# Performance work log

Hardware: AMD Instinct MI355X
Metric: run time of the kernel (lower is better)

## Reference

```python
import jax, jax.numpy as jnp
import numpy as np

S_GRID = 14.0
L_COORD = 5.0
L_NOOBJ = 0.5
B = 2


def _xywh2xyxy(b):
    # b: [..., 4] with (x, y, w, h); x,y are divided by S per the original module
    xy = b[..., :2] / S_GRID
    wh = b[..., 2:4]
    return jnp.concatenate([xy - 0.5 * wh, xy + 0.5 * wh], axis=-1)


def setup_inputs() -> dict:
    key = jax.random.key(0)
    k1, k2, k3, k4 = jax.random.split(key, 4)
    N, S, C = 4096, 14, 20
    pred_tensor = jax.random.uniform(k1, (N, S, S, B * 5 + C), dtype=jnp.float32, minval=0.05, maxval=1.0)
    target_boxes = jax.random.uniform(k2, (N, S, S, 4), dtype=jnp.float32, minval=0.05, maxval=1.0)
    target_cls = jax.random.normal(k3, (N, S, S, C), dtype=jnp.float32)
    has_object_map = jax.random.randint(k4, (N, S, S), 0, 2).astype(jnp.bool_)
    return {"pred_tensor": pred_tensor, "target_boxes": target_boxes,
            "target_cls": target_cls, "has_object_map": has_object_map}


def reference(pred_tensor, target_boxes, target_cls, has_object_map):
    N = pred_tensor.shape[0]
    mask = has_object_map                      # [N,S,S] bool
    maskf = mask.astype(pred_tensor.dtype)
    pb = pred_tensor[..., :B * 5].reshape(*pred_tensor.shape[:3], B, 5)  # [N,S,S,B,5]
    pc = pred_tensor[..., B * 5:]              # [N,S,S,20]

    # class loss: masked sum of squared errors over classes
    cls_loss = jnp.sum(maskf * jnp.sum((target_cls - pc) ** 2, axis=-1))

    # no-object loss: conf^2 on cells without objects, summed over both boxes
    conf = pb[..., 4]                          # [N,S,S,B]
    no_obj_loss = L_NOOBJ * jnp.sum(jnp.where(~mask[..., None], conf, 0.0) ** 2)

    # per-cell IoU of target vs each of the B predicted boxes (diag of original NxM)
    t_xyxy = _xywh2xyxy(target_boxes)          # [N,S,S,4]
    p_xyxy = _xywh2xyxy(pb[..., :4])           # [N,S,S,B,4]
    lt = jnp.maximum(t_xyxy[..., None, :2], p_xyxy[..., :2])
    rb = jnp.minimum(t_xyxy[..., None, 2:], p_xyxy[..., 2:])
    wh = jnp.clip(rb - lt, 0.0)
    inter = wh[..., 0] * wh[..., 1]            # [N,S,S,B]
    area_t = (t_xyxy[..., 2] - t_xyxy[..., 0]) * (t_xyxy[..., 3] - t_xyxy[..., 1])
    area_p = (p_xyxy[..., 2] - p_xyxy[..., 0]) * (p_xyxy[..., 3] - p_xyxy[..., 1])
    iou = inter / (area_t[..., None] + area_p - inter)  # [N,S,S,B]

    best_iou = jnp.max(iou, axis=-1)           # [N,S,S]
    best_idx = jnp.argmax(iou, axis=-1)        # [N,S,S]
    best_box = jnp.take_along_axis(pb, best_idx[..., None, None], axis=3)[..., 0, :]  # [N,S,S,5]

    xy_diff = jnp.where(mask[..., None], best_box[..., :2] - target_boxes[..., :2], 0.0)
    wh_p = jnp.where(mask[..., None], best_box[..., 2:4], 1.0)
    wh_t = jnp.where(mask[..., None], target_boxes[..., 2:4], 1.0)
    reg_loss = L_COORD * (jnp.sum(xy_diff ** 2)
                          + jnp.sum((jnp.sqrt(wh_p) - jnp.sqrt(wh_t)) ** 2))

    # containing-object confidence loss: mse(best_iou, best_box_conf) on object cells
    containing_obj_loss = jnp.sum(jnp.where(mask, best_iou - best_box[..., 4], 0.0) ** 2)

    total_loss = (cls_loss + no_obj_loss + reg_loss + containing_obj_loss) / N
    return (total_loss, reg_loss, containing_obj_loss, no_obj_loss, cls_loss)
```

## Files before the change

### kernel.cpp

```cpp
#include <hip/hip_runtime.h>
#include <math.h>


#define BLOCK 256
#define WPB 4
#define CPW 64

__global__ __launch_bounds__(BLOCK) void k_yolo(
    const float*  __restrict__ pred,
    const float4* __restrict__ tbox4,
    const float4* __restrict__ tcls4,
    const int*    __restrict__ mask,
    float4*       __restrict__ partial,
    int n_cells)
{
    __shared__ float sp[WPB][CPW * 30];
    const int tid  = threadIdx.x;
    const int lane = tid & 63;
    const int w    = tid >> 6;
    const long long cell0 = ((long long)blockIdx.x * WPB + w) * CPW;

    float cls = 0.f, noobj = 0.f, reg = 0.f, cont = 0.f;

    int mflag = 0;
    if (cell0 < n_cells) {
        const float4* p4 = reinterpret_cast<const float4*>(pred + cell0 * 30);
        float4* s4 = reinterpret_cast<float4*>(sp[w]);
        #pragma unroll
        for (int i = 0; i < 8; ++i) {
            int k = lane + i * 64;
            if (k < 480) s4[k] = p4[k];
        }
        long long cell = cell0 + lane;
        if (cell < (long long)n_cells) mflag = mask[cell];
    }
    __syncthreads();

    if (cell0 + lane < (long long)n_cells) {
        const float2* pc2 = reinterpret_cast<const float2*>(sp[w] + lane * 30);
        float2 v0 = pc2[0], v1 = pc2[1], v2 = pc2[2], v3 = pc2[3], v4 = pc2[4];
        float4 tb = tbox4[cell0 + lane];
        if (mflag) {
            float txc = tb.x / 14.0f, tyc = tb.y / 14.0f;
            float t0 = txc - 0.5f * tb.z, t1 = tyc - 0.5f * tb.w;
            float t2 = txc + 0.5f * tb.z, t3 = tyc + 0.5f * tb.w;
            float area_t = (t2 - t0) * (t3 - t1);
            float bx[2] = { v0.x, v2.y }, by[2] = { v0.y, v3.x };
            float bw[2] = { v1.x, v3.y }, bh[2] = { v1.y, v4.x };
            float bcf[2] = { v2.x, v4.y };
            float iou[2];
            #pragma unroll
            for (int b = 0; b < 2; ++b) {
                float px = bx[b] / 14.0f, py = by[b] / 14.0f;
                float q0 = px - 0.5f * bw[b], q1 = py - 0.5f * bh[b];
                float q2 = px + 0.5f * bw[b], q3 = py + 0.5f * bh[b];
                float lt0 = fmaxf(t0, q0), lt1 = fmaxf(t1, q1);
                float rb0 = fminf(t2, q2), rb1 = fminf(t3, q3);
                float ww = fmaxf(rb0 - lt0, 0.f), hh = fmaxf(rb1 - lt1, 0.f);
                float inter = ww * hh;
                float area_p = (q2 - q0) * (q3 - q1);
                iou[b] = inter / (area_t + area_p - inter);
            }
            int bi = (iou[1] > iou[0]) ? 1 : 0;
            float dx = bx[bi] - tb.x, dy = by[bi] - tb.y;
            float swd = sqrtf(bw[bi]) - sqrtf(tb.z);
            float shd = sqrtf(bh[bi]) - sqrtf(tb.w);
            reg = 5.0f * (dx*dx + dy*dy + swd*swd + shd*shd);
            float dco = iou[bi] - bcf[bi];
            cont = dco * dco;
        } else {
            noobj = 0.5f * (v2.x * v2.x + v4.y * v4.y);
        }
    }

    if (cell0 < n_cells) {
        const float4* t4 = tcls4 + cell0 * 5;
        #pragma unroll
        for (int i = 0; i < 5; ++i) {
            int j = lane + i * 64;
            int c = j / 5;
            int q = j - 5 * c;
            int mc = __shfl(mflag, c, 64);
            if (mc) {
                float4 t = t4[j];
                const float2* s2 = reinterpret_cast<const float2*>(sp[w] + c * 30 + 10 + q * 4);
                float2 a = s2[0], b = s2[1];
                float d0 = t.x - a.x, d1 = t.y - a.y;
                float d2 = t.z - b.x, d3 = t.w - b.y;
                cls += d0*d0 + d1*d1 + d2*d2 + d3*d3;
            }
        }
    }

    #pragma unroll
    for (int off = 32; off; off >>= 1) {
        cls   += __shfl_down(cls,   off, 64);
        noobj += __shfl_down(noobj, off, 64);
        reg   += __shfl_down(reg,   off, 64);
        cont  += __shfl_down(cont,  off, 64);
    }
    __shared__ float4 swr[WPB];
    if (lane == 0) swr[w] = make_float4(cls, noobj, reg, cont);
    __syncthreads();
    if (tid == 0) {
        float4 a = swr[0];
        #pragma unroll
        for (int i = 1; i < WPB; ++i) {
            float4 b = swr[i];
            a.x += b.x; a.y += b.y; a.z += b.z; a.w += b.w;
        }
        partial[blockIdx.x] = a;
    }
}

__global__ __launch_bounds__(BLOCK) void k_final(
    const float4* __restrict__ partial, int nblocks,
    float* __restrict__ out, float invN)
{
    float4 acc = make_float4(0.f, 0.f, 0.f, 0.f);
    for (int b = threadIdx.x; b < nblocks; b += BLOCK) {
        float4 v = partial[b];
        acc.x += v.x; acc.y += v.y; acc.z += v.z; acc.w += v.w;
    }
    #pragma unroll
    for (int off = 32; off; off >>= 1) {
        acc.x += __shfl_down(acc.x, off, 64);
        acc.y += __shfl_down(acc.y, off, 64);
        acc.z += __shfl_down(acc.z, off, 64);
        acc.w += __shfl_down(acc.w, off, 64);
    }
    __shared__ float4 sw[WPB];
    int lane = threadIdx.x & 63, w = threadIdx.x >> 6;
    if (lane == 0) sw[w] = acc;
    __syncthreads();
    if (threadIdx.x == 0) {
        float cls = 0.f, noobj = 0.f, reg = 0.f, cont = 0.f;
        #pragma unroll
        for (int i = 0; i < WPB; ++i) {
            cls += sw[i].x; noobj += sw[i].y; reg += sw[i].z; cont += sw[i].w;
        }
        out[0] = (cls + noobj + reg + cont) * invN;
        out[1] = reg;
        out[2] = cont;
        out[3] = noobj;
        out[4] = cls;
    }
}

extern "C" void kernel_launch(void* const* d_in, const int* in_sizes, int n_in,
                              void* d_out, int out_size, void* d_ws, size_t ws_size,
                              hipStream_t stream) {
    const float*  pred  = (const float*)d_in[0];
    const float4* tbox4 = (const float4*)d_in[1];
    const float4* tcls4 = (const float4*)d_in[2];
    const int*    mask  = (const int*)d_in[3];
    float* out = (float*)d_out;
    float4* partial = (float4*)d_ws;

    int n_cells = in_sizes[3];
    int N = in_sizes[0] / (14 * 14 * 30);
    int nblocks = (n_cells + BLOCK - 1) / BLOCK;

    hipLaunchKernelGGL(k_yolo, dim3(nblocks), dim3(BLOCK), 0, stream,
                       pred, tbox4, tcls4, mask, partial, n_cells);
    hipLaunchKernelGGL(k_final, dim3(1), dim3(BLOCK), 0, stream,
                       partial, nblocks, out, 1.0f / (float)N);
}
```

Measured before the change: 202.0 us.

## Stream pred and class targets as float2 in registers, stage only box fields in LDS

Each wavefront loads the pred tile as coalesced float2 words and the matching target-class words at the same time. The class SSE is computed directly in registers with a ballot-derived mask instead of staging all 30 floats per cell in shared memory. Only the 10 box fields go to a padded LDS region (stride 11), and the block-wide barrier is replaced by a waitcnt plus a compiler fence. The per-cell branches become mask-multiplied arithmetic, and launch bounds now request higher occupancy. In exchange, all target-class data is read even for no-object cells, and the wave-local LDS sync depends on a raw waitcnt encoding.

Result: slower. 209.7 us (+3.8%).

```diff
diff --git a/kernel.cpp b/kernel.cpp
--- a/kernel.cpp
+++ b/kernel.cpp
@@ -5,91 +5,114 @@
 #define BLOCK 256
 #define WPB 4
 #define CPW 64
+#define CW  11
 
-__global__ __launch_bounds__(BLOCK) void k_yolo(
-    const float*  __restrict__ pred,
-    const float4* __restrict__ tbox4,
-    const float4* __restrict__ tcls4,
+typedef float vf4 __attribute__((ext_vector_type(4)));
+
+__global__ __launch_bounds__(BLOCK, 8) void k_yolo(
+    const float2* __restrict__ pred2,
+    const vf4*    __restrict__ tbox4,
+    const float2* __restrict__ tcls2,
     const int*    __restrict__ mask,
     float4*       __restrict__ partial,
     int n_cells)
 {
-    __shared__ float sp[WPB][CPW * 30];
+    __shared__ float  sbox[WPB][CPW * CW];
+    __shared__ float4 swr[WPB];
     const int tid  = threadIdx.x;
     const int lane = tid & 63;
     const int w    = tid >> 6;
-    const long long cell0 = ((long long)blockIdx.x * WPB + w) * CPW;
+    const long long nc     = n_cells;
+    const long long ntiles = (nc + CPW - 1) / CPW;
+    const long long g      = (long long)blockIdx.x * WPB + w;
+    const long long cell0  = g * CPW;
+    long long gt   = (g < ntiles) ? g : (ntiles - 1);
+    long long base = gt * CPW;
+    if (base + CPW > nc) base = nc - CPW;
+    if (base < 0) base = 0;
 
-    float cls = 0.f, noobj = 0.f, reg = 0.f, cont = 0.f;
+    float* sb = &sbox[w][0];
 
-    int mflag = 0;
-    if (cell0 < n_cells) {
-        const float4* p4 = reinterpret_cast<const float4*>(pred + cell0 * 30);
-        float4* s4 = reinterpret_cast<float4*>(sp[w]);
+    int mraw = mask[base + lane];
+    vf4 tb   = tbox4[base + lane];
+    const bool vf    = (cell0 + (long long)lane) < nc;
+    const int  mflag = vf ? mraw : 0;
+    const float mff  = (float)mflag;
+    const float vff  = vf ? 1.0f : 0.0f;
+    const unsigned long long mbits = __ballot(mflag != 0);
+
+    float cls = 0.f;
+    const float2* pbase = pred2 + base * 15;
+    const float2* cbase = tcls2 + base * 10;
+
+    #pragma unroll
+    for (int h = 0; h < 2; ++h) {
+        const int i0 = (h == 0) ? 0 : 8;
+        const int in = (h == 0) ? 8 : 7;
+        float2 p2[8], t2[8];
         #pragma unroll
         for (int i = 0; i < 8; ++i) {
-            int k = lane + i * 64;
-            if (k < 480) s4[k] = p4[k];
+            if (i >= in) break;
+            int j = lane + 64 * (i0 + i);
+            int c = j / 15, r = j - 15 * c;
+            p2[i] = pbase[j];
+            int off = (r >= 5) ? (r - 5) : 0;
+            t2[i] = cbase[c * 10 + off];
         }
-        long long cell = cell0 + lane;
-        if (cell < (long long)n_cells) mflag = mask[cell];
-    }
-    __syncthreads();
-
-    if (cell0 + lane < (long long)n_cells) {
-        const float2* pc2 = reinterpret_cast<const float2*>(sp[w] + lane * 30);
-        float2 v0 = pc2[0], v1 = pc2[1], v2 = pc2[2], v3 = pc2[3], v4 = pc2[4];
-        float4 tb = tbox4[cell0 + lane];
-        if (mflag) {
-            float txc = tb.x / 14.0f, tyc = tb.y / 14.0f;
-            float t0 = txc - 0.5f * tb.z, t1 = tyc - 0.5f * tb.w;
-            float t2 = txc + 0.5f * tb.z, t3 = tyc + 0.5f * tb.w;
-            float area_t = (t2 - t0) * (t3 - t1);
-            float bx[2] = { v0.x, v2.y }, by[2] = { v0.y, v3.x };
-            float bw[2] = { v1.x, v3.y }, bh[2] = { v1.y, v4.x };
-            float bcf[2] = { v2.x, v4.y };
-            float iou[2];
-            #pragma unroll
-            for (int b = 0; b < 2; ++b) {
-                float px = bx[b] / 14.0f, py = by[b] / 14.0f;
-                float q0 = px - 0.5f * bw[b], q1 = py - 0.5f * bh[b];
-                float q2 = px + 0.5f * bw[b], q3 = py + 0.5f * bh[b];
-                float lt0 = fmaxf(t0, q0), lt1 = fmaxf(t1, q1);
-                float rb0 = fminf(t2, q2), rb1 = fminf(t3, q3);
-                float ww = fmaxf(rb0 - lt0, 0.f), hh = fmaxf(rb1 - lt1, 0.f);
-                float inter = ww * hh;
-                float area_p = (q2 - q0) * (q3 - q1);
-                iou[b] = inter / (area_t + area_p - inter);
+        #pragma unroll
+        for (int i = 0; i < 8; ++i) {
+            if (i >= in) break;
+            int j = lane + 64 * (i0 + i);
+            int c = j / 15, r = j - 15 * c;
+            if (r < 5) {
+                sb[c * CW + r * 2]     = p2[i].x;
+                sb[c * CW + r * 2 + 1] = p2[i].y;
+            } else {
+                float keep = ((((mbits >> c) & 1ull) != 0ull) &&
+                              (cell0 + (long long)c < nc)) ? 1.0f : 0.0f;
+                float d0 = t2[i].x - p2[i].x, d1 = t2[i].y - p2[i].y;
+                cls += keep * (d0 * d0 + d1 * d1);
             }
-            int bi = (iou[1] > iou[0]) ? 1 : 0;
-            float dx = bx[bi] - tb.x, dy = by[bi] - tb.y;
-            float swd = sqrtf(bw[bi]) - sqrtf(tb.z);
-            float shd = sqrtf(bh[bi]) - sqrtf(tb.w);
-            reg = 5.0f * (dx*dx + dy*dy + swd*swd + shd*shd);
-            float dco = iou[bi] - bcf[bi];
-            cont = dco * dco;
-        } else {
-            noobj = 0.5f * (v2.x * v2.x + v4.y * v4.y);
         }
     }
 
-    if (cell0 < n_cells) {
-        const float4* t4 = tcls4 + cell0 * 5;
+    __builtin_amdgcn_s_waitcnt(0xC07F);
+    __asm__ volatile("" ::: "memory");
+
+    float p[10];
+    #pragma unroll
+    for (int k = 0; k < 10; ++k) p[k] = sb[lane * CW + k];
+
+    float noobj, reg, cont;
+    {
+        float txc = tb.x / 14.0f, tyc = tb.y / 14.0f;
+        float t0 = txc - 0.5f * tb.z, t1 = tyc - 0.5f * tb.w;
+        float t2_ = txc + 0.5f * tb.z, t3 = tyc + 0.5f * tb.w;
+        float area_t = (t2_ - t0) * (t3 - t1);
+        float bx[2] = { p[0], p[5] }, by[2] = { p[1], p[6] };
+        float bw[2] = { p[2], p[7] }, bh[2] = { p[3], p[8] };
+        float bcf[2] = { p[4], p[9] };
+        float iou[2];
         #pragma unroll
-        for (int i = 0; i < 5; ++i) {
-            int j = lane + i * 64;
-            int c = j / 5;
-            int q = j - 5 * c;
-            int mc = __shfl(mflag, c, 64);
-            if (mc) {
-                float4 t = t4[j];
-                const float2* s2 = reinterpret_cast<const float2*>(sp[w] + c * 30 + 10 + q * 4);
-                float2 a = s2[0], b = s2[1];
-                float d0 = t.x - a.x, d1 = t.y - a.y;
-                float d2 = t.z - b.x, d3 = t.w - b.y;
-                cls += d0*d0 + d1*d1 + d2*d2 + d3*d3;
-            }
+        for (int b = 0; b < 2; ++b) {
+            float px = bx[b] / 14.0f, py = by[b] / 14.0f;
+            float q0 = px - 0.5f * bw[b], q1 = py - 0.5f * bh[b];
+            float q2 = px + 0.5f * bw[b], q3 = py + 0.5f * bh[b];
+            float lt0 = fmaxf(t0, q0), lt1 = fmaxf(t1, q1);
+            float rb0 = fminf(t2_, q2), rb1 = fminf(t3, q3);
+            float ww = fmaxf(rb0 - lt0, 0.f), hh = fmaxf(rb1 - lt1, 0.f);
+            float inter = ww * hh;
+            float area_p = (q2 - q0) * (q3 - q1);
+            iou[b] = inter / (area_t + area_p - inter);
         }
+        int bi = (iou[1] > iou[0]) ? 1 : 0;
+        float dx = bx[bi] - tb.x, dy = by[bi] - tb.y;
+        float swd = sqrtf(bw[bi]) - sqrtf(tb.z);
+        float shd = sqrtf(bh[bi]) - sqrtf(tb.w);
+        reg  = mff * 5.0f * (dx*dx + dy*dy + swd*swd + shd*shd);
+        float dco = iou[bi] - bcf[bi];
+        cont = mff * dco * dco;
+        noobj = (vff - mff) * 0.5f * (p[4] * p[4] + p[9] * p[9]);
     }
 
     #pragma unroll
@@ -99,7 +122,6 @@
         reg   += __shfl_down(reg,   off, 64);
         cont  += __shfl_down(cont,  off, 64);
     }
-    __shared__ float4 swr[WPB];
     if (lane == 0) swr[w] = make_float4(cls, noobj, reg, cont);
     __syncthreads();
     if (tid == 0) {
@@ -113,14 +135,14 @@
     }
 }
 
-__global__ __launch_bounds__(BLOCK) void k_final(
+__global__ __launch_bounds__(256) void k_final(
     const float4* __restrict__ partial, int nblocks,
     float* __restrict__ out, float invN)
 {
     float4 acc = make_float4(0.f, 0.f, 0.f, 0.f);
-    for (int b = threadIdx.x; b < nblocks; b += BLOCK) {
-        float4 v = partial[b];
-        acc.x += v.x; acc.y += v.y; acc.z += v.z; acc.w += v.w;
+    for (int b = threadIdx.x; b < nblocks; b += 256) {
+        float4 p = partial[b];
+        acc.x += p.x; acc.y += p.y; acc.z += p.z; acc.w += p.w;
     }
     #pragma unroll
     for (int off = 32; off; off >>= 1) {
@@ -129,14 +151,14 @@
         acc.z += __shfl_down(acc.z, off, 64);
         acc.w += __shfl_down(acc.w, off, 64);
     }
-    __shared__ float4 sw[WPB];
+    __shared__ float4 sw[4];
     int lane = threadIdx.x & 63, w = threadIdx.x >> 6;
     if (lane == 0) sw[w] = acc;
     __syncthreads();
     if (threadIdx.x == 0) {
         float cls = 0.f, noobj = 0.f, reg = 0.f, cont = 0.f;
         #pragma unroll
-        for (int i = 0; i < WPB; ++i) {
+        for (int i = 0; i < 4; ++i) {
             cls += sw[i].x; noobj += sw[i].y; reg += sw[i].z; cont += sw[i].w;
         }
         out[0] = (cls + noobj + reg + cont) * invN;
@@ -150,19 +172,20 @@
 extern "C" void kernel_launch(void* const* d_in, const int* in_sizes, int n_in,
                               void* d_out, int out_size, void* d_ws, size_t ws_size,
                               hipStream_t stream) {
-    const float*  pred  = (const float*)d_in[0];
-    const float4* tbox4 = (const float4*)d_in[1];
-    const float4* tcls4 = (const float4*)d_in[2];
+    const float2* pred2 = (const float2*)d_in[0];
+    const vf4*    tbox4 = (const vf4*)d_in[1];
+    const float2* tcls2 = (const float2*)d_in[2];
     const int*    mask  = (const int*)d_in[3];
     float* out = (float*)d_out;
     float4* partial = (float4*)d_ws;
 
     int n_cells = in_sizes[3];
     int N = in_sizes[0] / (14 * 14 * 30);
-    int nblocks = (n_cells + BLOCK - 1) / BLOCK;
+    long long ntiles = (n_cells + CPW - 1) / CPW;
+    int nblocks = (int)((ntiles + WPB - 1) / WPB);
 
     hipLaunchKernelGGL(k_yolo, dim3(nblocks), dim3(BLOCK), 0, stream,
-                       pred, tbox4, tcls4, mask, partial, n_cells);
-    hipLaunchKernelGGL(k_final, dim3(1), dim3(BLOCK), 0, stream,
+                       pred2, tbox4, tcls2, mask, partial, n_cells);
+    hipLaunchKernelGGL(k_final, dim3(1), dim3(256), 0, stream,
                        partial, nblocks, out, 1.0f / (float)N);
 }
```
